# Kernel optimization log

Measured on AMD Instinct MI355X. Metric: run time of the kernel, lower is better.

## Reference

```python
import jax, jax.numpy as jnp
import numpy as np

B, S, HID = 1, 2048, 2048
H = 16
DN, DR, DV = 128, 64, 128          # qk_nope_head_dim, qk_rope_head_dim, v_head_dim
DQ = DN + DR                        # q_head_dim = 192
QLR, KVLR = 1536, 512               # q_lora_rank, kv_lora_rank
MAXP = 32 * 1024
SCALE = DQ ** -0.5
EPS = 1e-6


def rmsnorm(x, w):
    return x * jax.lax.rsqrt(jnp.mean(x * x, axis=-1, keepdims=True) + EPS) * w


def rotate_half(x):
    h = x.shape[-1] // 2
    return jnp.concatenate((-x[..., h:], x[..., :h]), axis=-1)


def interleave_to_half(x):
    # torch: view(b,h,s,d//2,2).transpose(4,3).reshape(b,h,s,d)
    b, h, s, d = x.shape
    return x.reshape(b, h, s, d // 2, 2).transpose(0, 1, 2, 4, 3).reshape(b, h, s, d)


def setup_inputs() -> dict:
    key = jax.random.key(0)
    ks = jax.random.split(key, 8)
    def w(k, shape):
        fan_in = shape[-1]
        return jax.random.normal(k, shape, jnp.float32) * (fan_in ** -0.5)
    inp = {
        "hidden_states": jax.random.normal(ks[0], (B, S, HID), jnp.float32),
        "q_a_w": w(ks[1], (QLR, HID)),
        "q_a_ln": jnp.ones((QLR,), jnp.float32),
        "q_b_w": w(ks[2], (H * DQ, QLR)),
        "kv_a_w": w(ks[3], (KVLR + DR, HID)),
        "kv_a_ln": jnp.ones((KVLR,), jnp.float32),
        "kv_b_w": w(ks[4], (H * (DN + DV), KVLR)),
        "o_w": w(ks[5], (HID, H * DV)),
    }
    # rotary tables, seq_len = 32k
    inv_freq = 1.0 / (10000.0 ** (np.arange(0, DR, 2, dtype=np.float32) / DR))
    t = np.arange(MAXP, dtype=np.float32)
    freqs = np.outer(t, inv_freq)
    emb = np.concatenate((freqs, freqs), axis=-1)
    inp["cos"] = jnp.asarray(np.cos(emb), jnp.float32)
    inp["sin"] = jnp.asarray(np.sin(emb), jnp.float32)
    # bool mask, True = masked (causal)
    inp["attention_mask"] = jnp.triu(jnp.ones((S, S), bool), 1)[None, None]
    inp["position_ids"] = jnp.arange(S, dtype=jnp.int64 if jax.config.jax_enable_x64 else jnp.int32)[None].repeat(B, 0)
    return inp


def reference(hidden_states, q_a_w, q_a_ln, q_b_w, kv_a_w, kv_a_ln, kv_b_w, o_w,
              cos, sin, attention_mask, position_ids):
    b, s, _ = hidden_states.shape
    # low-rank Q: q_b(LN(q_a(x)))
    q = rmsnorm(hidden_states @ q_a_w.T, q_a_ln) @ q_b_w.T         # [b,s,H*DQ]
    q = q.reshape(b, s, H, DQ).transpose(0, 2, 1, 3)               # [b,H,s,DQ]
    q_nope, q_pe = q[..., :DN], q[..., DN:]
    # compressed KV + decoupled rope key
    ckv = hidden_states @ kv_a_w.T                                  # [b,s,KVLR+DR]
    compressed_kv, k_pe = ckv[..., :KVLR], ckv[..., KVLR:]
    k_pe = k_pe.reshape(b, s, 1, DR).transpose(0, 2, 1, 3)          # [b,1,s,DR]
    kv = rmsnorm(compressed_kv, kv_a_ln) @ kv_b_w.T                 # [b,s,H*(DN+DV)]
    kv = kv.reshape(b, s, H, DN + DV).transpose(0, 2, 1, 3)         # [b,H,s,DN+DV]
    k_nope, value_states = kv[..., :DN], kv[..., DN:]
    # rotary with interleaved->half reorder on the rope slice only
    cos_p = cos[position_ids][:, None]                              # [b,1,s,DR]
    sin_p = sin[position_ids][:, None]
    q_pe = interleave_to_half(q_pe)
    k_pe = interleave_to_half(k_pe)
    q_pe = q_pe * cos_p + rotate_half(q_pe) * sin_p
    k_pe = k_pe * cos_p + rotate_half(k_pe) * sin_p
    query_states = jnp.concatenate((q_nope, q_pe), axis=-1)         # [b,H,s,DQ]
    key_states = jnp.concatenate(
        (k_nope, jnp.broadcast_to(k_pe, (b, H, s, DR))), axis=-1)   # [b,H,s,DQ]
    # manual attention
    scores = jnp.einsum("bhqd,bhkd->bhqk", query_states, key_states) * SCALE
    scores = jnp.where(attention_mask, jnp.float32(-10000.0), scores)
    attn = jax.nn.softmax(scores.astype(jnp.float32), axis=-1).astype(query_states.dtype)
    attn_out = jnp.einsum("bhqk,bhkd->bhqd", attn, value_states)    # [b,H,s,DV]
    attn_out = attn_out.transpose(0, 2, 1, 3).reshape(b, s, H * DV)
    return attn_out @ o_w.T                                         # [b,s,HID]
```

## Files before the change

kernel.cpp:

```cpp
#include <hip/hip_runtime.h>
#include <stdint.h>

typedef unsigned short u16;
typedef __attribute__((ext_vector_type(8))) short short8;
typedef __attribute__((ext_vector_type(4))) float f32x4;
typedef __attribute__((ext_vector_type(4))) unsigned short ushort4_t;
typedef __attribute__((ext_vector_type(4))) float float4_t;

#define DEV_INLINE __device__ __forceinline__

DEV_INLINE u16 f2bf(float f) {
    union { float f; unsigned u; } x; x.f = f;
    unsigned u = x.u;
    unsigned r = (u + 0x7FFFu + ((u >> 16) & 1u)) >> 16;
    return (u16)r;
}

DEV_INLINE float bf2f(u16 b) {
    union { unsigned u; float f; } x; x.u = ((unsigned)b) << 16;
    return x.f;
}

DEV_INLINE float fexp2(float x) {
    float r;
    asm("v_exp_f32 %0, %1" : "=v"(r) : "v"(x));
    return r;
}

DEV_INLINE unsigned cvtpk_bf16(float lo, float hi) {
    unsigned r;
    asm("v_cvt_pk_bf16_f32 %0, %1, %2" : "=v"(r) : "v"(lo), "v"(hi));
    return r;
}

template <int CTRL>
DEV_INLINE float dppmax(float x) {
    union { float f; int i; } u; u.f = x;
    int y = __builtin_amdgcn_update_dpp(u.i, u.i, CTRL, 0xf, 0xf, true);
    union { int i; float f; } v; v.i = y;
    return fmaxf(x, v.f);
}

DEV_INLINE float rmax16(float x) {
    x = dppmax<0xB1>(x);
    x = dppmax<0x4E>(x);
    x = dppmax<0x141>(x);
    x = dppmax<0x140>(x);
    return x;
}

__global__ void conv_multi(const float* __restrict__ s0, u16* __restrict__ d0, long e0,
                           const float* __restrict__ s1, u16* __restrict__ d1, long e1,
                           const float* __restrict__ s2, u16* __restrict__ d2, long e2,
                           const float* __restrict__ s3, u16* __restrict__ d3, long e3,
                           const float* __restrict__ s4, u16* __restrict__ d4, long e4) {
    long i = (long)blockIdx.x * 256 + threadIdx.x;
    const float* s; u16* d; long base;
    if      (i < e0) { s = s0; d = d0; base = 0; }
    else if (i < e1) { s = s1; d = d1; base = e0; }
    else if (i < e2) { s = s2; d = d2; base = e1; }
    else if (i < e3) { s = s3; d = d3; base = e2; }
    else if (i < e4) { s = s4; d = d4; base = e3; }
    else return;
    long j = i - base;
    float4_t v = ((const float4_t*)s)[j];
    ushort4_t o;
    o.x = f2bf(v.x); o.y = f2bf(v.y); o.z = f2bf(v.z); o.w = f2bf(v.w);
    ((ushort4_t*)d)[j] = o;
}

__global__ void conv_pad(const float* __restrict__ in, u16* __restrict__ out,
                         int rows_valid, long n4, int cols4) {
    long i = (long)blockIdx.x * blockDim.x + threadIdx.x;
    if (i >= n4) return;
    long row = i / cols4;
    ushort4_t o; o.x = 0; o.y = 0; o.z = 0; o.w = 0;
    if (row < rows_valid) {
        float4_t v = ((const float4_t*)in)[i];
        o.x = f2bf(v.x); o.y = f2bf(v.y); o.z = f2bf(v.z); o.w = f2bf(v.w);
    }
    ((ushort4_t*)out)[i] = o;
}

__global__ void add2_f32(const float* __restrict__ a, const float* __restrict__ b,
                         float* __restrict__ c, long n4) {
    long i = (long)blockIdx.x * 256 + threadIdx.x;
    if (i >= n4) return;
    float4_t x = ((const float4_t*)a)[i];
    float4_t y = ((const float4_t*)b)[i];
    x.x += y.x; x.y += y.y; x.z += y.z; x.w += y.w;
    ((float4_t*)c)[i] = x;
}

#define BK 32

DEV_INLINE void gload16(const u16* g, u16* l) {
    __builtin_amdgcn_global_load_lds((const __attribute__((address_space(1))) unsigned int*)g,
                                     (__attribute__((address_space(3))) unsigned int*)l,
                                     16, 0, 0);
}

template <typename OT>
__global__ __launch_bounds__(256) void gemm64_db(const u16* __restrict__ A, const u16* __restrict__ B,
                                                 OT* __restrict__ C, int M, int N, int K) {
    __shared__ u16 As[2][64 * BK];
    __shared__ u16 Bs[2][128 * BK];
    const int tid = threadIdx.x;
    const int wid = tid >> 6, lane = tid & 63;
    const int lm = lane & 15, lk = lane >> 4;
    const long bm = (long)blockIdx.y * 64, bn = (long)blockIdx.x * 128;

    f32x4 acc[4][2] = {};

    const int rowS = lane >> 2;
    const int colS = ((lane & 3) ^ ((lane >> 3) & 3)) * 8;
    const int cs = (lm >> 1) & 3;
    const u16* Ag = A + (bm + wid * 16 + rowS) * (long)K + colS;
    const u16* Bg = B + (bn + wid * 32 + rowS) * (long)K + colS;
    const int aoff = wid * 16 * BK;
    const int boff = wid * 32 * BK;

    gload16(Ag, &As[0][aoff]);
    gload16(Bg, &Bs[0][boff]);
    gload16(Bg + 16 * (long)K, &Bs[0][boff + 16 * BK]);
    __syncthreads();

    int cur = 0;
    for (int k0 = 0; k0 < K; k0 += BK) {
        if (k0 + BK < K) {
            gload16(Ag + k0 + BK, &As[cur ^ 1][aoff]);
            gload16(Bg + k0 + BK, &Bs[cur ^ 1][boff]);
            gload16(Bg + 16 * (long)K + k0 + BK, &Bs[cur ^ 1][boff + 16 * BK]);
        }
        short8 af[4], bfr[2];
#pragma unroll
        for (int m = 0; m < 4; ++m)
            af[m] = *(const short8*)&As[cur][(m * 16 + lm) * BK + (lk ^ cs) * 8];
#pragma unroll
        for (int n = 0; n < 2; ++n)
            bfr[n] = *(const short8*)&Bs[cur][(wid * 32 + n * 16 + lm) * BK + (lk ^ cs) * 8];
#pragma unroll
        for (int m = 0; m < 4; ++m)
#pragma unroll
            for (int n = 0; n < 2; ++n)
                acc[m][n] = __builtin_amdgcn_mfma_f32_16x16x32_bf16(af[m], bfr[n], acc[m][n], 0, 0, 0);
        __syncthreads();
        cur ^= 1;
    }

#pragma unroll
    for (int m = 0; m < 4; ++m)
#pragma unroll
        for (int n = 0; n < 2; ++n)
#pragma unroll
            for (int r = 0; r < 4; ++r) {
                long idx = (bm + m * 16 + lk * 4 + r) * (long)N + bn + wid * 32 + n * 16 + lm;
                if constexpr (sizeof(OT) == 4) C[idx] = acc[m][n][r];
                else                           C[idx] = f2bf(acc[m][n][r]);
            }
}

template <typename OT, int SPLITK>
__global__ __launch_bounds__(256) void gemm128_db(const u16* __restrict__ A, const u16* __restrict__ B,
                                                  OT* __restrict__ C, int M, int N, int K) {
    __shared__ u16 As[2][128 * BK];
    __shared__ u16 Bs[2][128 * BK];
    const int tid = threadIdx.x;
    const int wid = tid >> 6, lane = tid & 63;
    const int lm = lane & 15, lk = lane >> 4;
    const int wr = wid >> 1, wc = wid & 1;
    const long bm = (long)blockIdx.y * 128, bn = (long)blockIdx.x * 128;
    const int Kh = K / SPLITK;
    const long kbase = (long)blockIdx.z * Kh;
    OT* Cp = C + (long)blockIdx.z * M * (long)N;

    f32x4 acc[4][4] = {};

    const int rowS = lane >> 2;
    const int colS = ((lane & 3) ^ ((lane >> 3) & 3)) * 8;
    const int cs = (lm >> 1) & 3;
    const u16* Ag = A + (bm + wid * 16 + rowS) * (long)K + kbase + colS;
    const u16* Bg = B + (bn + wid * 16 + rowS) * (long)K + kbase + colS;
    const int off0 = wid * 512;
    const int off1 = off0 + 64 * 32;

    gload16(Ag, &As[0][off0]);
    gload16(Ag + 64 * (long)K, &As[0][off1]);
    gload16(Bg, &Bs[0][off0]);
    gload16(Bg + 64 * (long)K, &Bs[0][off1]);
    __syncthreads();

    int cur = 0;
    for (int k0 = 0; k0 < Kh; k0 += BK) {
        if (k0 + BK < Kh) {
            gload16(Ag + k0 + BK, &As[cur ^ 1][off0]);
            gload16(Ag + 64 * (long)K + k0 + BK, &As[cur ^ 1][off1]);
            gload16(Bg + k0 + BK, &Bs[cur ^ 1][off0]);
            gload16(Bg + 64 * (long)K + k0 + BK, &Bs[cur ^ 1][off1]);
        }
        short8 af[4], bfr[4];
#pragma unroll
        for (int m = 0; m < 4; ++m)
            af[m] = *(const short8*)&As[cur][(wr * 64 + m * 16 + lm) * BK + (lk ^ cs) * 8];
#pragma unroll
        for (int n = 0; n < 4; ++n)
            bfr[n] = *(const short8*)&Bs[cur][(wc * 64 + n * 16 + lm) * BK + (lk ^ cs) * 8];
#pragma unroll
        for (int m = 0; m < 4; ++m)
#pragma unroll
            for (int n = 0; n < 4; ++n)
                acc[m][n] = __builtin_amdgcn_mfma_f32_16x16x32_bf16(af[m], bfr[n], acc[m][n], 0, 0, 0);
        __syncthreads();
        cur ^= 1;
    }

#pragma unroll
    for (int m = 0; m < 4; ++m)
#pragma unroll
        for (int n = 0; n < 4; ++n)
#pragma unroll
            for (int r = 0; r < 4; ++r) {
                long idx = (bm + wr * 64 + m * 16 + lk * 4 + r) * (long)N + bn + wc * 64 + n * 16 + lm;
                if constexpr (sizeof(OT) == 4) Cp[idx] = acc[m][n][r];
                else                           Cp[idx] = f2bf(acc[m][n][r]);
            }
}

__global__ __launch_bounds__(256) void rmsnorm_bf16(const float* __restrict__ in, const float* __restrict__ w,
                                                    u16* __restrict__ out, int ldin, int ldout, int ncols) {
    const int row = blockIdx.x, tid = threadIdx.x;
    const float* x = in + (long)row * ldin;
    float ss = 0.f;
    for (int c = tid; c < ncols; c += 256) { float v = x[c]; ss = fmaf(v, v, ss); }
#pragma unroll
    for (int off = 32; off > 0; off >>= 1) ss += __shfl_down(ss, off);
    __shared__ float part[4];
    if ((tid & 63) == 0) part[tid >> 6] = ss;
    __syncthreads();
    float tot = part[0] + part[1] + part[2] + part[3];
    float rs = rsqrtf(tot / (float)ncols + 1e-6f);
    for (int c = tid; c < ncols; c += 256) out[(long)row * ldout + c] = f2bf(x[c] * rs * w[c]);
}

__global__ void rope_k(const float* __restrict__ ckv, const int* __restrict__ pos,
                       const float* __restrict__ cosT, const float* __restrict__ sinT,
                       u16* __restrict__ Kb) {
    int idx = blockIdx.x * 256 + threadIdx.x;
    if (idx >= 2048 * 32) return;
    int s = idx >> 5, j = idx & 31;
    long p = pos[s];
    const float* row = ckv + (long)s * 2176 + 2048;
    float x0 = row[2 * j], x1 = row[2 * j + 1];
    float c0 = cosT[p * 64 + j],      s0 = sinT[p * 64 + j];
    float c1 = cosT[p * 64 + 32 + j], s1 = sinT[p * 64 + 32 + j];
    u16 o0 = f2bf(x0 * c0 - x1 * s0);
    u16 o1 = f2bf(x1 * c1 + x0 * s1);
#pragma unroll
    for (int h = 0; h < 16; ++h) {
        u16* kr = Kb + ((long)h * 2048 + s) * 192 + 128;
        kr[j] = o0; kr[32 + j] = o1;
    }
}

__global__ void build_q(const u16* __restrict__ q, const int* __restrict__ pos,
                        const float* __restrict__ cosT, const float* __restrict__ sinT,
                        u16* __restrict__ Qb) {
    long idx = (long)blockIdx.x * 256 + threadIdx.x;
    if (idx >= 16L * 2048 * 192) return;
    int d = (int)(idx % 192);
    int s = (int)((idx / 192) % 2048);
    int h = (int)(idx / (192L * 2048));
    const u16* qrow = q + (long)s * 3072 + h * 192;
    u16 outv;
    if (d < 128) {
        outv = qrow[d];
    } else {
        long p = pos[s];
        int dd = d - 128;
        float cv = cosT[p * 64 + dd], sv = sinT[p * 64 + dd];
        float val;
        if (dd < 32) val = bf2f(qrow[128 + 2 * dd]) * cv - bf2f(qrow[128 + 2 * dd + 1]) * sv;
        else { int jj = dd - 32; val = bf2f(qrow[128 + 2 * jj + 1]) * cv + bf2f(qrow[128 + 2 * jj]) * sv; }
        outv = f2bf(val);
    }
    Qb[((long)h * 2048 + s) * 192 + d] = outv;
}

__global__ __launch_bounds__(256) void build_kv2(const u16* __restrict__ kv, u16* __restrict__ Kb,
                                                 u16* __restrict__ Vt) {
    __shared__ u16 Ls[128][72];
    const int h = blockIdx.y, s0 = blockIdx.x * 64;
    const int tid = threadIdx.x;
#pragma unroll
    for (int i = 0; i < 8; ++i) {
        int u = i * 256 + tid;
        int r = u >> 5, c8 = (u & 31) * 8;
        short8 x = *(const short8*)(kv + (long)(s0 + r) * 4096 + h * 256 + c8);
        if (c8 < 128) {
            *(short8*)(Kb + ((long)h * 2048 + s0 + r) * 192 + c8) = x;
        } else {
#pragma unroll
            for (int j = 0; j < 8; ++j) {
                int d = c8 - 128 + j;
                Ls[d][r ^ (((d >> 3) & 7) << 3)] = (u16)x[j];
            }
        }
    }
    __syncthreads();
#pragma unroll
    for (int i = 0; i < 8; ++i) {
        int u = i * 256 + tid;
        int d = u >> 4, s4 = (u & 15) * 4;
        int swz = ((d >> 3) & 7) << 3;
        ushort4_t v;
        v.x = Ls[d][(s4 + 0) ^ swz]; v.y = Ls[d][(s4 + 1) ^ swz];
        v.z = Ls[d][(s4 + 2) ^ swz]; v.w = Ls[d][(s4 + 3) ^ swz];
        *(ushort4_t*)(Vt + ((long)h * 128 + d) * 2048 + s0 + s4) = v;
    }
}

__global__ __launch_bounds__(512) void attn_fwd(const u16* __restrict__ Qb, const u16* __restrict__ Kb,
                                                const u16* __restrict__ Vt, u16* __restrict__ Ao) {
    __shared__ __align__(16) char smem[92672];

    const int b = blockIdx.x;
    const int h = (b & 7) * 2 + ((b >> 3) & 1);
    const int pi = b >> 4;
    const int tid = threadIdx.x;
    const int wid = tid >> 6, lane = tid & 63;
    const int lm = lane & 15, lk = lane >> 4;
    const int s = wid >> 2, wp = wid & 3;
    const int t256 = tid & 255;

    u16* Ks0 = (u16*)smem + s * 12288;
    u16* Vs0 = (u16*)(smem + 49152) + s * 8192;
    u16* PsW = (u16*)(smem + 81920) + wid * 640;
    float* ML = (float*)(smem + 92160);
    float* Ob = (float*)smem;

    const u16* Kh = Kb + (long)h * 2048 * 192;
    const u16* Vh = Vt + (long)h * 128 * 2048;

    short8 bones = {};
    if (lm == 0) {
#pragma unroll
        for (int j = 0; j < 8; ++j) bones[j] = (short)0x3F80;
    }
    const float C2 = 0.104117548f;

    for (int half = 0; half < 2; ++half) {
        const int qi = half ? (31 - pi) : pi;
        const int q0 = qi * 64;
        const int nt = 2 * qi + 2;
        const int niter = qi + 1;

        short8 qf[6];
        const u16* qbase = Qb + ((long)h * 2048 + q0 + wp * 16 + lm) * 192;
#pragma unroll
        for (int kf = 0; kf < 6; ++kf) qf[kf] = *(const short8*)(qbase + kf * 32 + lk * 8);

        f32x4 o[8] = {};
        f32x4 o9 = {};
        float mrow[4] = {-1e30f, -1e30f, -1e30f, -1e30f};

        short8 kreg[3], vreg[2];
        {
            const long k0 = s * 32;
#pragma unroll
            for (int i = 0; i < 3; ++i) {
                int idx = i * 256 + t256; int r = idx / 24, c = (idx % 24) * 8;
                kreg[i] = *(const short8*)(Kh + (k0 + r) * 192 + c);
            }
#pragma unroll
            for (int i = 0; i < 2; ++i) {
                int idx = i * 256 + t256; int dv = idx >> 2, kvb = idx & 3;
                vreg[i] = *(const short8*)(Vh + (long)dv * 2048 + k0 + kvb * 8);
            }
#pragma unroll
            for (int i = 0; i < 3; ++i) {
                int idx = i * 256 + t256; int r = idx / 24, c8 = idx % 24;
                *(short8*)&Ks0[r * 192 + ((c8 ^ (r & 7)) << 3)] = kreg[i];
            }
#pragma unroll
            for (int i = 0; i < 2; ++i) {
                int idx = i * 256 + t256; int dv = idx >> 2, kvb = idx & 3;
                *(short8*)&Vs0[kvb * 1024 + ((dv * 8) ^ (kvb * 16))] = vreg[i];
            }
        }
        __syncthreads();

        int cur = 0;
        for (int it = 0; it < niter; ++it) {
            const int ts = 2 * it + s;
            const int k0 = ts * 32;
            const bool more = (it + 1 < niter);

            if (more) {
                const long k0n = (long)(ts + 2) * 32;
#pragma unroll
                for (int i = 0; i < 3; ++i) {
                    int idx = i * 256 + t256; int r = idx / 24, c = (idx % 24) * 8;
                    kreg[i] = *(const short8*)(Kh + (k0n + r) * 192 + c);
                }
#pragma unroll
                for (int i = 0; i < 2; ++i) {
                    int idx = i * 256 + t256; int dv = idx >> 2, kvb = idx & 3;
                    vreg[i] = *(const short8*)(Vh + (long)dv * 2048 + k0n + kvb * 8);
                }
            }

            const u16* KsC = Ks0 + cur * 6144;
            const u16* VsC = Vs0 + cur * 4096;

            f32x4 sfr[2] = {};
#pragma unroll
            for (int n = 0; n < 2; ++n)
#pragma unroll
                for (int kf = 0; kf < 6; ++kf) {
                    short8 kb = *(const short8*)&KsC[(n * 16 + lm) * 192 + (((kf * 4 + lk) ^ (lm & 7)) << 3)];
                    sfr[n] = __builtin_amdgcn_mfma_f32_16x16x32_bf16(qf[kf], kb, sfr[n], 0, 0, 0);
                }

            float sv[2][4];
            const bool bt = (ts >= nt - 2);
#pragma unroll
            for (int n = 0; n < 2; ++n)
#pragma unroll
                for (int r = 0; r < 4; ++r) {
                    float val = sfr[n][r] * C2;
                    if (bt && (k0 + n * 16 + lm > q0 + wp * 16 + lk * 4 + r)) val = -1e30f;
                    sv[n][r] = val;
                }

            float pmax[4];
#pragma unroll
            for (int r = 0; r < 4; ++r)
                pmax[r] = rmax16(fmaxf(sv[0][r], sv[1][r]));
            bool need = (pmax[0] > mrow[0] + 8.f) || (pmax[1] > mrow[1] + 8.f) ||
                        (pmax[2] > mrow[2] + 8.f) || (pmax[3] > mrow[3] + 8.f);
            if (__any(need)) {
#pragma unroll
                for (int r = 0; r < 4; ++r) {
                    float mnew = fmaxf(mrow[r], pmax[r]);
                    float alpha = fexp2(mrow[r] - mnew);
                    mrow[r] = mnew;
#pragma unroll
                    for (int d = 0; d < 8; ++d) o[d][r] *= alpha;
                    o9[r] *= alpha;
                }
            }
#pragma unroll
            for (int n = 0; n < 2; ++n) {
                float p0 = fexp2(sv[n][0] - mrow[0]);
                float p1 = fexp2(sv[n][1] - mrow[1]);
                float p2 = fexp2(sv[n][2] - mrow[2]);
                float p3 = fexp2(sv[n][3] - mrow[3]);
                unsigned pk01 = cvtpk_bf16(p0, p1);
                unsigned pk23 = cvtpk_bf16(p2, p3);
                int rb = (lk * 4) * 40 + n * 16 + lm;
                PsW[rb]       = (u16)pk01;
                PsW[rb + 40]  = (u16)(pk01 >> 16);
                PsW[rb + 80]  = (u16)pk23;
                PsW[rb + 120] = (u16)(pk23 >> 16);
            }

            short8 pf = *(const short8*)&PsW[lm * 40 + lk * 8];
#pragma unroll
            for (int d = 0; d < 8; ++d) {
                short8 vf = *(const short8*)&VsC[lk * 1024 + (((d * 16 + lm) * 8) ^ (lk * 16))];
                o[d] = __builtin_amdgcn_mfma_f32_16x16x32_bf16(pf, vf, o[d], 0, 0, 0);
            }
            o9 = __builtin_amdgcn_mfma_f32_16x16x32_bf16(pf, bones, o9, 0, 0, 0);

            if (more) {
                u16* KsN = Ks0 + (cur ^ 1) * 6144;
                u16* VsN = Vs0 + (cur ^ 1) * 4096;
#pragma unroll
                for (int i = 0; i < 3; ++i) {
                    int idx = i * 256 + t256; int r = idx / 24, c8 = idx % 24;
                    *(short8*)&KsN[r * 192 + ((c8 ^ (r & 7)) << 3)] = kreg[i];
                }
#pragma unroll
                for (int i = 0; i < 2; ++i) {
                    int idx = i * 256 + t256; int dv = idx >> 2, kvb = idx & 3;
                    *(short8*)&VsN[kvb * 1024 + ((dv * 8) ^ (kvb * 16))] = vreg[i];
                }
            }
            __syncthreads();
            cur ^= 1;
        }

        if (s == 1) {
#pragma unroll
            for (int d = 0; d < 8; ++d)
#pragma unroll
                for (int r = 0; r < 4; ++r)
                    Ob[(wp * 16 + lk * 4 + r) * 128 + d * 16 + lm] = o[d][r];
            if (lm == 0) {
#pragma unroll
                for (int r = 0; r < 4; ++r) {
                    int row = wp * 16 + lk * 4 + r;
                    ML[row * 2 + 0] = mrow[r];
                    ML[row * 2 + 1] = o9[r];
                }
            }
        }
        __syncthreads();
        if (s == 0) {
            float e0[4], e1[4], invl[4];
#pragma unroll
            for (int r = 0; r < 4; ++r) {
                int row = wp * 16 + lk * 4 + r;
                float m1 = ML[row * 2 + 0];
                float l1 = ML[row * 2 + 1];
                float l0 = __shfl(o9[r], lane & 48);
                float M = fmaxf(mrow[r], m1);
                e0[r] = fexp2(mrow[r] - M);
                e1[r] = fexp2(m1 - M);
                invl[r] = 1.f / (l0 * e0[r] + l1 * e1[r]);
            }
#pragma unroll
            for (int d = 0; d < 8; ++d)
#pragma unroll
                for (int r = 0; r < 4; ++r) {
                    int row = wp * 16 + lk * 4 + r;
                    float val = (o[d][r] * e0[r] +
                                 Ob[row * 128 + d * 16 + lm] * e1[r]) * invl[r];
                    Ao[((long)q0 + row) * 2048 + h * 128 + d * 16 + lm] = f2bf(val);
                }
        }
        __syncthreads();
    }
}

extern "C" void kernel_launch(void* const* d_in, const int* in_sizes, int n_in,
                              void* d_out, int out_size, void* d_ws, size_t ws_size,
                              hipStream_t stream) {
    (void)in_sizes; (void)n_in; (void)out_size; (void)ws_size;
    const float* hidden  = (const float*)d_in[0];
    const float* q_a_w   = (const float*)d_in[1];
    const float* q_a_ln  = (const float*)d_in[2];
    const float* q_b_w   = (const float*)d_in[3];
    const float* kv_a_w  = (const float*)d_in[4];
    const float* kv_a_ln = (const float*)d_in[5];
    const float* kv_b_w  = (const float*)d_in[6];
    const float* o_w     = (const float*)d_in[7];
    const float* cosT    = (const float*)d_in[8];
    const float* sinT    = (const float*)d_in[9];
    const int*   pos     = (const int*)d_in[11];

    char* ws = (char*)d_ws;
    u16* o_w_bf   = (u16*)(ws + 0);
    u16* qb_w_bf  = (u16*)(ws + 8388608);
    u16* kvb_w_bf = (u16*)(ws + 17825792);
    u16* qn_bf    = (u16*)(ws + 22020096);
    u16* kvn_bf   = (u16*)(ws + 28311552);
    u16* Qb       = (u16*)(ws + 30408704);
    u16* Kb       = (u16*)(ws + 42991616);
    u16* Vt       = (u16*)(ws + 55574528);
    u16* aout_bf  = (u16*)(ws + 63963136);
    u16*   hid_bf    = (u16*)(ws + 72351744);
    u16*   qkva_w_bf = (u16*)(ws + 80740352);
    float* qkva_f    = (float*)(ws + 89653248);
    u16*   q_f_bf    = (u16*)(ws + 72351744);
    u16*   kv_f_bf   = (u16*)(ws + 89653248);
    float* op0       = (float*)(ws + 107479040);
    float* op1       = (float*)(ws + 124256256);

    conv_multi<<<17920, 256, 0, stream>>>(
        hidden, hid_bf,    1048576L,
        q_a_w,  qkva_w_bf, 1835008L,
        q_b_w,  qb_w_bf,   3014656L,
        kv_b_w, kvb_w_bf,  3538944L,
        o_w,    o_w_bf,    4587520L);
    conv_pad<<<(640L*2048/4 + 255)/256, 256, 0, stream>>>(kv_a_w, qkva_w_bf + 1536L*2048, 576, 640L*2048/4, 512);

    gemm64_db<float><<<dim3(17, 32), 256, 0, stream>>>(hid_bf, qkva_w_bf, qkva_f, 2048, 2176, 2048);

    rmsnorm_bf16<<<2048, 256, 0, stream>>>(qkva_f, q_a_ln, qn_bf, 2176, 1536, 1536);
    rmsnorm_bf16<<<2048, 256, 0, stream>>>(qkva_f + 1536, kv_a_ln, kvn_bf, 2176, 512, 512);
    rope_k<<<(2048*32)/256, 256, 0, stream>>>(qkva_f, pos, cosT, sinT, Kb);

    gemm128_db<u16, 1><<<dim3(24, 16), 256, 0, stream>>>(qn_bf, qb_w_bf, q_f_bf, 2048, 3072, 1536);
    gemm128_db<u16, 1><<<dim3(32, 16), 256, 0, stream>>>(kvn_bf, kvb_w_bf, kv_f_bf, 2048, 4096, 512);

    build_q<<<(unsigned)((16L*2048*192 + 255)/256), 256, 0, stream>>>(q_f_bf, pos, cosT, sinT, Qb);
    build_kv2<<<dim3(32, 16), 256, 0, stream>>>(kv_f_bf, Kb, Vt);

    attn_fwd<<<256, 512, 0, stream>>>(Qb, Kb, Vt, aout_bf);

    gemm128_db<float, 2><<<dim3(16, 16, 2), 256, 0, stream>>>(aout_bf, o_w_bf, op0, 2048, 2048, 2048);
    add2_f32<<<4096, 256, 0, stream>>>(op0, op1, (float*)d_out, 2048L*2048/4);
}
```

Baseline: 248.7 us.

## Fuse Q/KV up-projections with RoPE epilogue and drop split-K output reduction

The separate q_b and kv_b GEMMs are merged into one launch using 64x128 tiles, and the query RoPE and head-major scatter now happen in the GEMM epilogue. Partner lanes are exchanged with a DPP xor-1 swap, which removes the build_q pass and its intermediate buffer. RoPE now keeps the interleaved pair order in both Q and K rather than reordering to half layout. That is valid because the same permutation is applied to both sides of the dot product. The output projection now writes straight to the output with the 64-row GEMM, dropping the split-K partials and the add kernel, at the cost of a scattered, less coalesced Q store and per-element cos/sin loads in the epilogue.

```diff
diff --git a/kernel.cpp b/kernel.cpp
--- a/kernel.cpp
+++ b/kernel.cpp
@@ -34,18 +34,25 @@
 }
 
 template <int CTRL>
-DEV_INLINE float dppmax(float x) {
+DEV_INLINE float dppmaxf(float x) {
     union { float f; int i; } u; u.f = x;
     int y = __builtin_amdgcn_update_dpp(u.i, u.i, CTRL, 0xf, 0xf, true);
     union { int i; float f; } v; v.i = y;
     return fmaxf(x, v.f);
 }
 
+DEV_INLINE float dpp_xor1(float x) {
+    union { float f; int i; } u; u.f = x;
+    int y = __builtin_amdgcn_update_dpp(u.i, u.i, 0xB1, 0xf, 0xf, true);
+    union { int i; float f; } v; v.i = y;
+    return v.f;
+}
+
 DEV_INLINE float rmax16(float x) {
-    x = dppmax<0xB1>(x);
-    x = dppmax<0x4E>(x);
-    x = dppmax<0x141>(x);
-    x = dppmax<0x140>(x);
+    x = dppmaxf<0xB1>(x);
+    x = dppmaxf<0x4E>(x);
+    x = dppmaxf<0x141>(x);
+    x = dppmaxf<0x140>(x);
     return x;
 }
 
@@ -82,16 +89,6 @@
     ((ushort4_t*)out)[i] = o;
 }
 
-__global__ void add2_f32(const float* __restrict__ a, const float* __restrict__ b,
-                         float* __restrict__ c, long n4) {
-    long i = (long)blockIdx.x * 256 + threadIdx.x;
-    if (i >= n4) return;
-    float4_t x = ((const float4_t*)a)[i];
-    float4_t y = ((const float4_t*)b)[i];
-    x.x += y.x; x.y += y.y; x.z += y.z; x.w += y.w;
-    ((float4_t*)c)[i] = x;
-}
-
 #define BK 32
 
 DEV_INLINE void gload16(const u16* g, u16* l) {
@@ -160,70 +157,100 @@
             }
 }
 
-template <typename OT, int SPLITK>
-__global__ __launch_bounds__(256) void gemm128_db(const u16* __restrict__ A, const u16* __restrict__ B,
-                                                  OT* __restrict__ C, int M, int N, int K) {
-    __shared__ u16 As[2][128 * BK];
+__global__ __launch_bounds__(256) void gemm_qkv(const u16* __restrict__ qnA, const u16* __restrict__ qbB,
+                                                const u16* __restrict__ kvnA, const u16* __restrict__ kvbB,
+                                                u16* __restrict__ Qb, u16* __restrict__ kvout,
+                                                const int* __restrict__ pos,
+                                                const float* __restrict__ cosT, const float* __restrict__ sinT) {
+    __shared__ u16 As[2][64 * BK];
     __shared__ u16 Bs[2][128 * BK];
     const int tid = threadIdx.x;
     const int wid = tid >> 6, lane = tid & 63;
     const int lm = lane & 15, lk = lane >> 4;
-    const int wr = wid >> 1, wc = wid & 1;
-    const long bm = (long)blockIdx.y * 128, bn = (long)blockIdx.x * 128;
-    const int Kh = K / SPLITK;
-    const long kbase = (long)blockIdx.z * Kh;
-    OT* Cp = C + (long)blockIdx.z * M * (long)N;
-
-    f32x4 acc[4][4] = {};
+
+    const bool isq = blockIdx.x < 768;
+    const int gx = isq ? blockIdx.x : blockIdx.x - 768;
+    const int nb = isq ? 24 : 32;
+    const int K  = isq ? 1536 : 512;
+    const u16* A = isq ? qnA : kvnA;
+    const u16* B = isq ? qbB : kvbB;
+    const long bn = (long)(gx % nb) * 128;
+    const long bm = (long)(gx / nb) * 64;
+
+    f32x4 acc[4][2] = {};
 
     const int rowS = lane >> 2;
     const int colS = ((lane & 3) ^ ((lane >> 3) & 3)) * 8;
     const int cs = (lm >> 1) & 3;
-    const u16* Ag = A + (bm + wid * 16 + rowS) * (long)K + kbase + colS;
-    const u16* Bg = B + (bn + wid * 16 + rowS) * (long)K + kbase + colS;
-    const int off0 = wid * 512;
-    const int off1 = off0 + 64 * 32;
-
-    gload16(Ag, &As[0][off0]);
-    gload16(Ag + 64 * (long)K, &As[0][off1]);
-    gload16(Bg, &Bs[0][off0]);
-    gload16(Bg + 64 * (long)K, &Bs[0][off1]);
+    const u16* Ag = A + (bm + wid * 16 + rowS) * (long)K + colS;
+    const u16* Bg = B + (bn + wid * 32 + rowS) * (long)K + colS;
+    const int aoff = wid * 16 * BK;
+    const int boff = wid * 32 * BK;
+
+    gload16(Ag, &As[0][aoff]);
+    gload16(Bg, &Bs[0][boff]);
+    gload16(Bg + 16 * (long)K, &Bs[0][boff + 16 * BK]);
     __syncthreads();
 
     int cur = 0;
-    for (int k0 = 0; k0 < Kh; k0 += BK) {
-        if (k0 + BK < Kh) {
-            gload16(Ag + k0 + BK, &As[cur ^ 1][off0]);
-            gload16(Ag + 64 * (long)K + k0 + BK, &As[cur ^ 1][off1]);
-            gload16(Bg + k0 + BK, &Bs[cur ^ 1][off0]);
-            gload16(Bg + 64 * (long)K + k0 + BK, &Bs[cur ^ 1][off1]);
-        }
-        short8 af[4], bfr[4];
+    for (int k0 = 0; k0 < K; k0 += BK) {
+        if (k0 + BK < K) {
+            gload16(Ag + k0 + BK, &As[cur ^ 1][aoff]);
+            gload16(Bg + k0 + BK, &Bs[cur ^ 1][boff]);
+            gload16(Bg + 16 * (long)K + k0 + BK, &Bs[cur ^ 1][boff + 16 * BK]);
+        }
+        short8 af[4], bfr[2];
 #pragma unroll
         for (int m = 0; m < 4; ++m)
-            af[m] = *(const short8*)&As[cur][(wr * 64 + m * 16 + lm) * BK + (lk ^ cs) * 8];
-#pragma unroll
-        for (int n = 0; n < 4; ++n)
-            bfr[n] = *(const short8*)&Bs[cur][(wc * 64 + n * 16 + lm) * BK + (lk ^ cs) * 8];
+            af[m] = *(const short8*)&As[cur][(m * 16 + lm) * BK + (lk ^ cs) * 8];
+#pragma unroll
+        for (int n = 0; n < 2; ++n)
+            bfr[n] = *(const short8*)&Bs[cur][(wid * 32 + n * 16 + lm) * BK + (lk ^ cs) * 8];
 #pragma unroll
         for (int m = 0; m < 4; ++m)
 #pragma unroll
-            for (int n = 0; n < 4; ++n)
+            for (int n = 0; n < 2; ++n)
                 acc[m][n] = __builtin_amdgcn_mfma_f32_16x16x32_bf16(af[m], bfr[n], acc[m][n], 0, 0, 0);
         __syncthreads();
         cur ^= 1;
     }
 
-#pragma unroll
-    for (int m = 0; m < 4; ++m)
-#pragma unroll
-        for (int n = 0; n < 4; ++n)
-#pragma unroll
-            for (int r = 0; r < 4; ++r) {
-                long idx = (bm + wr * 64 + m * 16 + lk * 4 + r) * (long)N + bn + wc * 64 + n * 16 + lm;
-                if constexpr (sizeof(OT) == 4) Cp[idx] = acc[m][n][r];
-                else                           Cp[idx] = f2bf(acc[m][n][r]);
-            }
+    if (!isq) {
+#pragma unroll
+        for (int m = 0; m < 4; ++m)
+#pragma unroll
+            for (int n = 0; n < 2; ++n)
+#pragma unroll
+                for (int r = 0; r < 4; ++r) {
+                    long idx = (bm + m * 16 + lk * 4 + r) * 4096L + bn + wid * 32 + n * 16 + lm;
+                    kvout[idx] = f2bf(acc[m][n][r]);
+                }
+    } else {
+#pragma unroll
+        for (int n = 0; n < 2; ++n) {
+            const int c = (int)bn + wid * 32 + n * 16 + lm;
+            const int h = c / 192;
+            const int d = c - h * 192;
+            const bool pe = (d >= 128);
+            const int t = (d - 128) >> 1;
+#pragma unroll
+            for (int m = 0; m < 4; ++m)
+#pragma unroll
+                for (int r = 0; r < 4; ++r) {
+                    const long row = bm + m * 16 + lk * 4 + r;
+                    float own = acc[m][n][r];
+                    float par = dpp_xor1(own);
+                    float val = own;
+                    if (pe) {
+                        long p = pos[row];
+                        float cc = cosT[p * 64 + t];
+                        float ss = sinT[p * 64 + t];
+                        val = (d & 1) ? own * cc + par * ss : own * cc - par * ss;
+                    }
+                    Qb[((long)h * 2048 + row) * 192 + d] = f2bf(val);
+                }
+        }
+    }
 }
 
 __global__ __launch_bounds__(256) void rmsnorm_bf16(const float* __restrict__ in, const float* __restrict__ w,
@@ -251,39 +278,14 @@
     long p = pos[s];
     const float* row = ckv + (long)s * 2176 + 2048;
     float x0 = row[2 * j], x1 = row[2 * j + 1];
-    float c0 = cosT[p * 64 + j],      s0 = sinT[p * 64 + j];
-    float c1 = cosT[p * 64 + 32 + j], s1 = sinT[p * 64 + 32 + j];
+    float c0 = cosT[p * 64 + j], s0 = sinT[p * 64 + j];
     u16 o0 = f2bf(x0 * c0 - x1 * s0);
-    u16 o1 = f2bf(x1 * c1 + x0 * s1);
+    u16 o1 = f2bf(x1 * c0 + x0 * s0);
 #pragma unroll
     for (int h = 0; h < 16; ++h) {
         u16* kr = Kb + ((long)h * 2048 + s) * 192 + 128;
-        kr[j] = o0; kr[32 + j] = o1;
-    }
-}
-
-__global__ void build_q(const u16* __restrict__ q, const int* __restrict__ pos,
-                        const float* __restrict__ cosT, const float* __restrict__ sinT,
-                        u16* __restrict__ Qb) {
-    long idx = (long)blockIdx.x * 256 + threadIdx.x;
-    if (idx >= 16L * 2048 * 192) return;
-    int d = (int)(idx % 192);
-    int s = (int)((idx / 192) % 2048);
-    int h = (int)(idx / (192L * 2048));
-    const u16* qrow = q + (long)s * 3072 + h * 192;
-    u16 outv;
-    if (d < 128) {
-        outv = qrow[d];
-    } else {
-        long p = pos[s];
-        int dd = d - 128;
-        float cv = cosT[p * 64 + dd], sv = sinT[p * 64 + dd];
-        float val;
-        if (dd < 32) val = bf2f(qrow[128 + 2 * dd]) * cv - bf2f(qrow[128 + 2 * dd + 1]) * sv;
-        else { int jj = dd - 32; val = bf2f(qrow[128 + 2 * jj + 1]) * cv + bf2f(qrow[128 + 2 * jj]) * sv; }
-        outv = f2bf(val);
-    }
-    Qb[((long)h * 2048 + s) * 192 + d] = outv;
+        kr[2 * j] = o0; kr[2 * j + 1] = o1;
+    }
 }
 
 __global__ __launch_bounds__(256) void build_kv2(const u16* __restrict__ kv, u16* __restrict__ Kb,
@@ -562,10 +564,7 @@
     u16*   hid_bf    = (u16*)(ws + 72351744);
     u16*   qkva_w_bf = (u16*)(ws + 80740352);
     float* qkva_f    = (float*)(ws + 89653248);
-    u16*   q_f_bf    = (u16*)(ws + 72351744);
-    u16*   kv_f_bf   = (u16*)(ws + 89653248);
-    float* op0       = (float*)(ws + 107479040);
-    float* op1       = (float*)(ws + 124256256);
+    u16*   kv_f_bf   = (u16*)(ws + 107479040);
 
     conv_multi<<<17920, 256, 0, stream>>>(
         hidden, hid_bf,    1048576L,
@@ -581,14 +580,11 @@
     rmsnorm_bf16<<<2048, 256, 0, stream>>>(qkva_f + 1536, kv_a_ln, kvn_bf, 2176, 512, 512);
     rope_k<<<(2048*32)/256, 256, 0, stream>>>(qkva_f, pos, cosT, sinT, Kb);
 
-    gemm128_db<u16, 1><<<dim3(24, 16), 256, 0, stream>>>(qn_bf, qb_w_bf, q_f_bf, 2048, 3072, 1536);
-    gemm128_db<u16, 1><<<dim3(32, 16), 256, 0, stream>>>(kvn_bf, kvb_w_bf, kv_f_bf, 2048, 4096, 512);
-
-    build_q<<<(unsigned)((16L*2048*192 + 255)/256), 256, 0, stream>>>(q_f_bf, pos, cosT, sinT, Qb);
+    gemm_qkv<<<1792, 256, 0, stream>>>(qn_bf, qb_w_bf, kvn_bf, kvb_w_bf, Qb, kv_f_bf, pos, cosT, sinT);
+
     build_kv2<<<dim3(32, 16), 256, 0, stream>>>(kv_f_bf, Kb, Vt);
 
     attn_fwd<<<256, 512, 0, stream>>>(Qb, Kb, Vt, aout_bf);
 
-    gemm128_db<float, 2><<<dim3(16, 16, 2), 256, 0, stream>>>(aout_bf, o_w_bf, op0, 2048, 2048, 2048);
-    add2_f32<<<4096, 256, 0, stream>>>(op0, op1, (float*)d_out, 2048L*2048/4);
-}
+    gemm64_db<float><<<dim3(16, 32), 256, 0, stream>>>(aout_bf, o_w_bf, (float*)d_out, 2048, 2048, 2048);
+}
```

Result: faster. 235.8 us (-5.2%).
